# Kernel tuning notes

Measured on AMD Instinct MI355X. Metric: run time of the kernel, lower is better.

## Reference

```python
import jax, jax.numpy as jnp
import numpy as np

B, N, I, D, K = 64, 16, 2048, 32, 32  # batch, num_capsule, input_num_capsule, dim_capsule, input_dim_capsule
ROUTINGS = 3
EPS = 1e-07


def squash(s):
    # squared_norm includes per-element eps before the sum, matching torch code
    sq = jnp.sum(s * s + EPS, axis=-1, keepdims=True)
    return sq * s / ((1.0 + sq) * jnp.sqrt(sq))


def setup_inputs() -> dict:
    key = jax.random.key(0)
    kx, kw = jax.random.split(key)
    x = jax.random.normal(kx, (B, I, K), dtype=jnp.float32)
    # xavier_uniform over a [N, I, D, K] tensor: fan_in = D*K (last two dims treated as matrix by torch init? torch treats dim1.. as fan) -- use gain=1 uniform bound per torch's convention: fan_in = I*D*K/... Use simple xavier over (fan_in=K, fan_out=D) receptive field I*N.
    fan_in = I * K
    fan_out = I * D  # torch: fan_in = size(1)*receptive, here just use uniform bound from full-tensor xavier
    bound = float(np.sqrt(6.0 / (fan_in + fan_out)))
    W = jax.random.uniform(kw, (N, I, D, K), minval=-bound, maxval=bound, dtype=jnp.float32)
    return {"x": x, "W": W}


def reference(x, W):
    # u_hat[b,n,i,d] = sum_k W[n,i,d,k] * x[b,i,k]
    u_hat = jnp.einsum('nidk,bik->bnid', W, x)
    b = jnp.zeros((B, N, I), dtype=u_hat.dtype)
    v = None
    for r in range(ROUTINGS):
        c = jax.nn.softmax(b, axis=1)                 # softmax over num_capsule
        s = jnp.einsum('bni,bnid->bnd', c, u_hat)     # [B, N, D]
        v = squash(s)
        if r < ROUTINGS - 1:
            a = jnp.einsum('bnid,bnd->bni', u_hat, v)
            b = b + a
    return v  # [B, N, D]
```

## Files before the change

### kernel.cpp

```cpp
#include <hip/hip_runtime.h>
#include <stdint.h>

#define Bdim 64
#define Ndim 16
#define Idim 2048
#define Ddim 32
#define Kdim 32
#define EPSV 1e-7f

#define TILE_I   4
#define TILES_PB 16
#define NB_Y     (Idim / (TILE_I * TILES_PB))

typedef __attribute__((ext_vector_type(8))) short short8v;
typedef __attribute__((ext_vector_type(4))) float f32x4;

static __device__ __forceinline__ unsigned pk_rne(float a, float b) {
    unsigned ua = __float_as_uint(a);
    unsigned ub = __float_as_uint(b);
    ua = (ua + 0x7fffu + ((ua >> 16) & 1u)) >> 16;
    ub = (ub + 0x7fffu + ((ub >> 16) & 1u)) >> 16;
    return (ua & 0xffffu) | (ub << 16);
}
static __device__ __forceinline__ float bf2f(unsigned us) {
    return __uint_as_float(us << 16);
}

#define GLL16(g, s)                                                              \
    __builtin_amdgcn_global_load_lds(                                            \
        (const __attribute__((address_space(1))) void*)(uintptr_t)(const void*)(g), \
        (__attribute__((address_space(3))) void*)(uintptr_t)(void*)(s), 16, 0, 0)

__global__ __launch_bounds__(256) void convert_x(
    const float* __restrict__ x, unsigned short* __restrict__ x2)
{
    const int i  = blockIdx.x;
    const int b  = threadIdx.x >> 2;
    const int ko = threadIdx.x & 3;
    const float* src = x + ((size_t)b * Idim + i) * Kdim + (ko << 3);
    float4 a = ((const float4*)src)[0];
    float4 c = ((const float4*)src)[1];
    uint4 o;
    o.x = pk_rne(a.x, a.y); o.y = pk_rne(a.z, a.w);
    o.z = pk_rne(c.x, c.y); o.w = pk_rne(c.z, c.w);
    *(uint4*)(x2 + ((size_t)i * 64 + b) * 32 + (ko << 3)) = o;
}

__global__ __launch_bounds__(256) void pass1_dma(
    const float* __restrict__ W, const unsigned short* __restrict__ x2,
    unsigned short* __restrict__ uhat, float* __restrict__ s0)
{
    __shared__ float          ldsW[2][TILE_I * 1024];
    __shared__ unsigned short ldsX[2][TILE_I * 2048];

    const int n     = blockIdx.x;
    const int iblk0 = blockIdx.y * (TILE_I * TILES_PB);
    const int tid   = threadIdx.x;
    const int l     = tid & 63;
    const int bcol  = ((tid >> 6) << 4) + (l & 15);
    const int krow  = l >> 4;

    const float*          Wblk = W  + ((size_t)n * Idim + iblk0) * (Ddim * Kdim);
    const unsigned short* Xblk = x2 + (size_t)iblk0 * (64 * 32);

    f32x4 acc0 = {0.f, 0.f, 0.f, 0.f};
    f32x4 acc1 = {0.f, 0.f, 0.f, 0.f};
    const f32x4 zero = {0.f, 0.f, 0.f, 0.f};

    auto stage = [&](int t, int buf) {
        const float* Wt = Wblk + (size_t)t * (TILE_I * 1024);
        float* dw = &ldsW[buf][0];
        #pragma unroll
        for (int j = 0; j < 4; ++j) {
            const int c  = j * 256 + tid;
            const int lc = c & 63, h = (c >> 6) & 1, mt = (c >> 7) & 1, il = c >> 8;
            const float* src = Wt + il * 1024 + ((mt << 4) + (lc & 15)) * 32
                                  + ((lc >> 4) << 3) + (h << 2);
            GLL16(src, dw + (size_t)c * 4);
        }
        const unsigned short* Xt = Xblk + (size_t)t * (TILE_I * 2048);
        unsigned short* dx = &ldsX[buf][0];
        #pragma unroll
        for (int j = 0; j < 4; ++j) {
            const int c = j * 256 + tid;
            GLL16(Xt + (size_t)c * 8, dx + (size_t)c * 8);
        }
    };

    stage(0, 0);

    for (int t = 0; t < TILES_PB; ++t) {
        if (t + 1 < TILES_PB) stage(t + 1, (t + 1) & 1);
        if (t == 0 || t == TILES_PB - 1) {
            asm volatile("s_waitcnt vmcnt(8)" ::: "memory");
        } else {
            asm volatile("s_waitcnt vmcnt(16)" ::: "memory");
        }
        __builtin_amdgcn_s_barrier();
        __builtin_amdgcn_sched_barrier(0);

        const float*          lw = &ldsW[t & 1][0];
        const unsigned short* lx = &ldsX[t & 1][0];
        const int ibase = iblk0 + t * TILE_I;

        #pragma unroll
        for (int il = 0; il < TILE_I; ++il) {
            const int i = ibase + il;

            union { short8v v; unsigned u[4]; } bf, af0, af1;
            bf.v = *(const short8v*)(lx + il * 2048 + bcol * 32 + (krow << 3));

            const float4 w00 = *(const float4*)(lw + ((il * 256 + l)       << 2));
            const float4 w01 = *(const float4*)(lw + ((il * 256 + 64 + l)  << 2));
            const float4 w10 = *(const float4*)(lw + ((il * 256 + 128 + l) << 2));
            const float4 w11 = *(const float4*)(lw + ((il * 256 + 192 + l) << 2));
            af0.u[0] = pk_rne(w00.x, w00.y); af0.u[1] = pk_rne(w00.z, w00.w);
            af0.u[2] = pk_rne(w01.x, w01.y); af0.u[3] = pk_rne(w01.z, w01.w);
            af1.u[0] = pk_rne(w10.x, w10.y); af1.u[1] = pk_rne(w10.z, w10.w);
            af1.u[2] = pk_rne(w11.x, w11.y); af1.u[3] = pk_rne(w11.z, w11.w);

            f32x4 c0 = __builtin_amdgcn_mfma_f32_16x16x32_bf16(af0.v, bf.v, zero, 0, 0, 0);
            f32x4 c1 = __builtin_amdgcn_mfma_f32_16x16x32_bf16(af1.v, bf.v, zero, 0, 0, 0);

            const size_t ubase = (((size_t)i * Ndim + n) * 64 + bcol) * Ddim + (krow << 2);
            uint2 p0; p0.x = pk_rne(c0[0], c0[1]); p0.y = pk_rne(c0[2], c0[3]);
            *(uint2*)(uhat + ubase) = p0;
            uint2 p1; p1.x = pk_rne(c1[0], c1[1]); p1.y = pk_rne(c1[2], c1[3]);
            *(uint2*)(uhat + ubase + 16) = p1;

            acc0 += c0;
            acc1 += c1;
        }
        asm volatile("s_waitcnt lgkmcnt(0)" ::: "memory");
        __builtin_amdgcn_s_barrier();
        __builtin_amdgcn_sched_barrier(0);
    }

    float* sp = s0 + ((size_t)bcol * Ndim + n) * Ddim + (krow << 2);
    #pragma unroll
    for (int r = 0; r < 4; ++r) atomicAdd(sp + r, acc0[r]);
    #pragma unroll
    for (int r = 0; r < 4; ++r) atomicAdd(sp + 16 + r, acc1[r]);
}

__global__ __launch_bounds__(256) void pass1_simple(
    const float* __restrict__ W, const float* __restrict__ x,
    unsigned short* __restrict__ uhat, float* __restrict__ s0, int bbase, int Bc)
{
    const int IB = 16;
    const int n  = blockIdx.x;
    const int i0 = blockIdx.y * IB;
    const int w  = threadIdx.x >> 6;
    const int l  = threadIdx.x & 63;
    const int bcol  = (w << 4) + (l & 15);
    const int bglob = bbase + bcol;
    const int krow  = l >> 4;

    f32x4 acc0 = {0.f,0.f,0.f,0.f}, acc1 = {0.f,0.f,0.f,0.f};
    const f32x4 zero = {0.f,0.f,0.f,0.f};

    for (int ii = 0; ii < IB; ++ii) {
        const int i = i0 + ii;
        const float* xp = x + ((size_t)bglob * Idim + i) * Kdim + (krow << 3);
        float4 xa = ((const float4*)xp)[0];
        float4 xb = ((const float4*)xp)[1];
        union { short8v v; unsigned u[4]; } bf, af0, af1;
        bf.u[0]=pk_rne(xa.x,xa.y); bf.u[1]=pk_rne(xa.z,xa.w);
        bf.u[2]=pk_rne(xb.x,xb.y); bf.u[3]=pk_rne(xb.z,xb.w);

        const float* wbase = W + ((size_t)n * Idim + i) * Ddim * Kdim + (krow << 3);
        const float* wp0 = wbase + (size_t)(l & 15) * Kdim;
        float4 wa = ((const float4*)wp0)[0];
        float4 wb = ((const float4*)wp0)[1];
        af0.u[0]=pk_rne(wa.x,wa.y); af0.u[1]=pk_rne(wa.z,wa.w);
        af0.u[2]=pk_rne(wb.x,wb.y); af0.u[3]=pk_rne(wb.z,wb.w);
        const float* wp1 = wp0 + 16 * Kdim;
        float4 wc = ((const float4*)wp1)[0];
        float4 wd = ((const float4*)wp1)[1];
        af1.u[0]=pk_rne(wc.x,wc.y); af1.u[1]=pk_rne(wc.z,wc.w);
        af1.u[2]=pk_rne(wd.x,wd.y); af1.u[3]=pk_rne(wd.z,wd.w);

        f32x4 c0 = __builtin_amdgcn_mfma_f32_16x16x32_bf16(af0.v, bf.v, zero, 0,0,0);
        f32x4 c1 = __builtin_amdgcn_mfma_f32_16x16x32_bf16(af1.v, bf.v, zero, 0,0,0);

        const size_t ubase = (((size_t)i * Ndim + n) * Bc + bcol) * Ddim + (krow << 2);
        uint2 p0; p0.x=pk_rne(c0[0],c0[1]); p0.y=pk_rne(c0[2],c0[3]);
        *(uint2*)(uhat + ubase) = p0;
        uint2 p1; p1.x=pk_rne(c1[0],c1[1]); p1.y=pk_rne(c1[2],c1[3]);
        *(uint2*)(uhat + ubase + 16) = p1;
        acc0 += c0; acc1 += c1;
    }
    float* sp = s0 + ((size_t)bglob * Ndim + n) * Ddim + (krow << 2);
    #pragma unroll
    for (int r = 0; r < 4; ++r) atomicAdd(sp + r, acc0[r]);
    #pragma unroll
    for (int r = 0; r < 4; ++r) atomicAdd(sp + 16 + r, acc1[r]);
}

template<int FIRST>
__global__ __launch_bounds__(256) void route_kernel(
    const unsigned short* __restrict__ uhat, const float* __restrict__ vin,
    float* __restrict__ bbuf, float* __restrict__ sout, int bbase, int Bc)
{
    const int bc = blockIdx.x;
    const int it = blockIdx.y;
    const int w = threadIdx.x >> 6;
    const int l = threadIdx.x & 63;
    const int g = l >> 2, q = l & 3;
    const int bglob = bbase + bc;

    const float* vp = vin + ((size_t)bglob * Ndim + g) * Ddim + (q << 3);
    float vreg[8];
    *(float4*)&vreg[0] = ((const float4*)vp)[0];
    *(float4*)&vreg[4] = ((const float4*)vp)[1];

    float sacc[8];
    #pragma unroll
    for (int j = 0; j < 8; ++j) sacc[j] = 0.f;

    for (int base = 0; base < 128; base += 16) {
        const int i0v = (it << 7) + base + w;

        uint4 ur[4];
        float bl[4];
        #pragma unroll
        for (int j = 0; j < 4; ++j) {
            const int i = i0v + 4 * j;
            ur[j] = *(const uint4*)(uhat + (((size_t)i * Ndim + g) * Bc + bc) * Ddim + (q << 3));
            if (!FIRST) bl[j] = bbuf[((size_t)bc * Idim + i) * Ndim + g];
        }

        #pragma unroll
        for (int j = 0; j < 4; ++j) {
            const int i = i0v + 4 * j;
            float u[8];
            u[0] = bf2f(ur[j].x & 0xffffu); u[1] = bf2f(ur[j].x >> 16);
            u[2] = bf2f(ur[j].y & 0xffffu); u[3] = bf2f(ur[j].y >> 16);
            u[4] = bf2f(ur[j].z & 0xffffu); u[5] = bf2f(ur[j].z >> 16);
            u[6] = bf2f(ur[j].w & 0xffffu); u[7] = bf2f(ur[j].w >> 16);

            float p = 0.f;
            #pragma unroll
            for (int k = 0; k < 8; ++k) p = fmaf(u[k], vreg[k], p);
            p += __shfl_xor(p, 1);
            p += __shfl_xor(p, 2);

            float logit = p;
            if (FIRST) {
                if (q == 0) bbuf[((size_t)bc * Idim + i) * Ndim + g] = p;
            } else {
                logit += bl[j];
            }
            float m = logit;
            m = fmaxf(m, __shfl_xor(m, 4));
            m = fmaxf(m, __shfl_xor(m, 8));
            m = fmaxf(m, __shfl_xor(m, 16));
            m = fmaxf(m, __shfl_xor(m, 32));
            float e = __expf(logit - m);
            float z = e;
            z += __shfl_xor(z, 4);
            z += __shfl_xor(z, 8);
            z += __shfl_xor(z, 16);
            z += __shfl_xor(z, 32);
            float c = e / z;

            #pragma unroll
            for (int k = 0; k < 8; ++k) sacc[k] = fmaf(c, u[k], sacc[k]);
        }
    }

    __shared__ float sl[4][512];
    #pragma unroll
    for (int j = 0; j < 8; ++j) sl[w][(l << 3) + j] = sacc[j];
    __syncthreads();
    for (int e2 = threadIdx.x; e2 < 512; e2 += 256) {
        float vsum = sl[0][e2] + sl[1][e2] + sl[2][e2] + sl[3][e2];
        atomicAdd(sout + (size_t)bglob * (Ndim * Ddim) + e2, vsum);
    }
}

__global__ __launch_bounds__(256) void squash_kernel(
    const float* __restrict__ s, float* __restrict__ vout, float scale, int bbase)
{
    const int tid = blockIdx.x * 256 + threadIdx.x;
    const int row = tid >> 5;
    const int d   = tid & 31;
    const size_t off = ((size_t)bbase * Ndim + row) * Ddim + d;
    float sv = s[off] * scale;
    float t = fmaf(sv, sv, EPSV);
    t += __shfl_xor(t, 1);
    t += __shfl_xor(t, 2);
    t += __shfl_xor(t, 4);
    t += __shfl_xor(t, 8);
    t += __shfl_xor(t, 16);
    float vv = sv * t / ((1.f + t) * sqrtf(t));
    vout[off] = vv;
}

extern "C" void kernel_launch(void* const* d_in, const int* in_sizes, int n_in,
                              void* d_out, int out_size, void* d_ws, size_t ws_size,
                              hipStream_t stream)
{
    (void)in_sizes; (void)n_in; (void)out_size;
    const float* x = (const float*)d_in[0];
    const float* W = (const float*)d_in[1];
    float* out = (float*)d_out;

    const size_t snd = (size_t)Bdim * Ndim * Ddim;
    const size_t fixed = 5 * snd * sizeof(float);

    int Bc = 64;
    while (Bc > 16) {
        size_t need = (size_t)Bc * Idim * Ndim * Ddim * 2 + (size_t)Bc * Idim * Ndim * 4 + fixed;
        if (need <= ws_size) break;
        Bc >>= 1;
    }

    char* p = (char*)d_ws;
    unsigned short* uhat = (unsigned short*)p; p += (size_t)Bc * Idim * Ndim * Ddim * 2;
    float* bbuf = (float*)p;                   p += (size_t)Bc * Idim * Ndim * 4;
    float* sbuf = (float*)p;
    float* s0 = sbuf;
    float* s1 = sbuf + snd;
    float* s2 = sbuf + 2 * snd;
    float* v0 = sbuf + 3 * snd;
    float* v1 = sbuf + 4 * snd;

    for (int bbase = 0; bbase < Bdim; bbase += Bc) {
        (void)hipMemsetAsync(sbuf, 0, 3 * snd * sizeof(float), stream);

        if (Bc == 64) {
            unsigned short* x2 = (unsigned short*)bbuf;
            convert_x<<<dim3(Idim), 256, 0, stream>>>(x, x2);
            pass1_dma<<<dim3(Ndim, NB_Y), 256, 0, stream>>>(W, x2, uhat, s0);
        } else {
            pass1_simple<<<dim3(Ndim, Idim / 16), dim3(64 * (Bc / 16)), 0, stream>>>(
                W, x, uhat, s0, bbase, Bc);
        }
        squash_kernel<<<dim3(Bc * 2), 256, 0, stream>>>(s0, v0, 1.f / 16.f, bbase);

        route_kernel<1><<<dim3(Bc, Idim / 128), 256, 0, stream>>>(uhat, v0, bbuf, s1, bbase, Bc);
        squash_kernel<<<dim3(Bc * 2), 256, 0, stream>>>(s1, v1, 1.f, bbase);

        route_kernel<0><<<dim3(Bc, Idim / 128), 256, 0, stream>>>(uhat, v1, bbuf, s2, bbase, Bc);
        squash_kernel<<<dim3(Bc * 2), 256, 0, stream>>>(s2, out, 1.f, bbase);
    }
}
```

Measured before the change: 175.6 us.

## Deepen pass1 DMA pipeline to four buffers and restructure routing thread mapping

The pass1 kernel now uses smaller i-tiles (2 instead of 4) with a four-deep LDS ring and three tiles of prefetch, adjusting the vmcnt waits to match. The aim is to hide more global-load latency per block. The routing kernel is remapped so each lane owns a whole capsule (all 32 d values) for one i. This removes the intra-quad dot-product shuffles and the max-reduction, drops the softmax max subtraction and swaps the division for a reciprocal. The trade-offs are higher register pressure (64+ floats per lane), wider per-lane loads and possible overflow in exp without max subtraction.

```diff
diff --git a/kernel.cpp b/kernel.cpp
--- a/kernel.cpp
+++ b/kernel.cpp
@@ -8,9 +8,10 @@
 #define Kdim 32
 #define EPSV 1e-7f
 
-#define TILE_I   4
-#define TILES_PB 16
+#define TILE_I   2
+#define TILES_PB 32
 #define NB_Y     (Idim / (TILE_I * TILES_PB))
+#define NBUF     4
 
 typedef __attribute__((ext_vector_type(8))) short short8v;
 typedef __attribute__((ext_vector_type(4))) float f32x4;
@@ -24,6 +25,12 @@
 }
 static __device__ __forceinline__ float bf2f(unsigned us) {
     return __uint_as_float(us << 16);
+}
+static __device__ __forceinline__ void unpack8(uint4 r, float* u) {
+    u[0] = bf2f(r.x & 0xffffu); u[1] = bf2f(r.x >> 16);
+    u[2] = bf2f(r.y & 0xffffu); u[3] = bf2f(r.y >> 16);
+    u[4] = bf2f(r.z & 0xffffu); u[5] = bf2f(r.z >> 16);
+    u[6] = bf2f(r.w & 0xffffu); u[7] = bf2f(r.w >> 16);
 }
 
 #define GLL16(g, s)                                                              \
@@ -50,8 +57,8 @@
     const float* __restrict__ W, const unsigned short* __restrict__ x2,
     unsigned short* __restrict__ uhat, float* __restrict__ s0)
 {
-    __shared__ float          ldsW[2][TILE_I * 1024];
-    __shared__ unsigned short ldsX[2][TILE_I * 2048];
+    __shared__ float          ldsW[NBUF][TILE_I * 1024];
+    __shared__ unsigned short ldsX[NBUF][TILE_I * 2048];
 
     const int n     = blockIdx.x;
     const int iblk0 = blockIdx.y * (TILE_I * TILES_PB);
@@ -67,11 +74,12 @@
     f32x4 acc1 = {0.f, 0.f, 0.f, 0.f};
     const f32x4 zero = {0.f, 0.f, 0.f, 0.f};
 
-    auto stage = [&](int t, int buf) {
+    auto stage = [&](int t) {
+        const int buf = t & (NBUF - 1);
         const float* Wt = Wblk + (size_t)t * (TILE_I * 1024);
         float* dw = &ldsW[buf][0];
         #pragma unroll
-        for (int j = 0; j < 4; ++j) {
+        for (int j = 0; j < 2; ++j) {
             const int c  = j * 256 + tid;
             const int lc = c & 63, h = (c >> 6) & 1, mt = (c >> 7) & 1, il = c >> 8;
             const float* src = Wt + il * 1024 + ((mt << 4) + (lc & 15)) * 32
@@ -81,26 +89,30 @@
         const unsigned short* Xt = Xblk + (size_t)t * (TILE_I * 2048);
         unsigned short* dx = &ldsX[buf][0];
         #pragma unroll
-        for (int j = 0; j < 4; ++j) {
+        for (int j = 0; j < 2; ++j) {
             const int c = j * 256 + tid;
             GLL16(Xt + (size_t)c * 8, dx + (size_t)c * 8);
         }
     };
 
-    stage(0, 0);
+    stage(0); stage(1); stage(2);
 
     for (int t = 0; t < TILES_PB; ++t) {
-        if (t + 1 < TILES_PB) stage(t + 1, (t + 1) & 1);
+        if (t + 3 < TILES_PB) stage(t + 3);
         if (t == 0 || t == TILES_PB - 1) {
-            asm volatile("s_waitcnt vmcnt(8)" ::: "memory");
+            asm volatile("s_waitcnt vmcnt(12)" ::: "memory");
+        } else if (t == 1 || t == TILES_PB - 2) {
+            asm volatile("s_waitcnt vmcnt(16)" ::: "memory");
+        } else if (t == 2 || t == TILES_PB - 3) {
+            asm volatile("s_waitcnt vmcnt(20)" ::: "memory");
         } else {
-            asm volatile("s_waitcnt vmcnt(16)" ::: "memory");
+            asm volatile("s_waitcnt vmcnt(24)" ::: "memory");
         }
         __builtin_amdgcn_s_barrier();
         __builtin_amdgcn_sched_barrier(0);
 
-        const float*          lw = &ldsW[t & 1][0];
-        const unsigned short* lx = &ldsX[t & 1][0];
+        const float*          lw = &ldsW[t & (NBUF - 1)][0];
+        const unsigned short* lx = &ldsX[t & (NBUF - 1)][0];
         const int ibase = iblk0 + t * TILE_I;
 
         #pragma unroll
@@ -204,78 +216,78 @@
 {
     const int bc = blockIdx.x;
     const int it = blockIdx.y;
-    const int w = threadIdx.x >> 6;
-    const int l = threadIdx.x & 63;
-    const int g = l >> 2, q = l & 3;
+    const int w  = threadIdx.x >> 6;
+    const int l  = threadIdx.x & 63;
+    const int g    = l & 15;
+    const int iloc = l >> 4;
     const int bglob = bbase + bc;
 
-    const float* vp = vin + ((size_t)bglob * Ndim + g) * Ddim + (q << 3);
-    float vreg[8];
-    *(float4*)&vreg[0] = ((const float4*)vp)[0];
-    *(float4*)&vreg[4] = ((const float4*)vp)[1];
-
-    float sacc[8];
-    #pragma unroll
-    for (int j = 0; j < 8; ++j) sacc[j] = 0.f;
-
-    for (int base = 0; base < 128; base += 16) {
-        const int i0v = (it << 7) + base + w;
-
-        uint4 ur[4];
-        float bl[4];
-        #pragma unroll
-        for (int j = 0; j < 4; ++j) {
-            const int i = i0v + 4 * j;
-            ur[j] = *(const uint4*)(uhat + (((size_t)i * Ndim + g) * Bc + bc) * Ddim + (q << 3));
-            if (!FIRST) bl[j] = bbuf[((size_t)bc * Idim + i) * Ndim + g];
-        }
-
-        #pragma unroll
-        for (int j = 0; j < 4; ++j) {
-            const int i = i0v + 4 * j;
-            float u[8];
-            u[0] = bf2f(ur[j].x & 0xffffu); u[1] = bf2f(ur[j].x >> 16);
-            u[2] = bf2f(ur[j].y & 0xffffu); u[3] = bf2f(ur[j].y >> 16);
-            u[4] = bf2f(ur[j].z & 0xffffu); u[5] = bf2f(ur[j].z >> 16);
-            u[6] = bf2f(ur[j].w & 0xffffu); u[7] = bf2f(ur[j].w >> 16);
-
-            float p = 0.f;
-            #pragma unroll
-            for (int k = 0; k < 8; ++k) p = fmaf(u[k], vreg[k], p);
-            p += __shfl_xor(p, 1);
-            p += __shfl_xor(p, 2);
-
-            float logit = p;
-            if (FIRST) {
-                if (q == 0) bbuf[((size_t)bc * Idim + i) * Ndim + g] = p;
-            } else {
-                logit += bl[j];
-            }
-            float m = logit;
-            m = fmaxf(m, __shfl_xor(m, 4));
-            m = fmaxf(m, __shfl_xor(m, 8));
-            m = fmaxf(m, __shfl_xor(m, 16));
-            m = fmaxf(m, __shfl_xor(m, 32));
-            float e = __expf(logit - m);
-            float z = e;
-            z += __shfl_xor(z, 4);
-            z += __shfl_xor(z, 8);
-            z += __shfl_xor(z, 16);
-            z += __shfl_xor(z, 32);
-            float c = e / z;
-
-            #pragma unroll
-            for (int k = 0; k < 8; ++k) sacc[k] = fmaf(c, u[k], sacc[k]);
-        }
+    float v[32];
+    {
+        const float* vp = vin + ((size_t)bglob * Ndim + g) * Ddim;
+        #pragma unroll
+        for (int r = 0; r < 8; ++r) *(float4*)&v[r * 4] = ((const float4*)vp)[r];
+    }
+
+    float sacc[32];
+    #pragma unroll
+    for (int d = 0; d < 32; ++d) sacc[d] = 0.f;
+
+    const int ibase0 = (it << 7) + (w << 5);
+    for (int j = 0; j < 8; ++j) {
+        const int i = ibase0 + (j << 2) + iloc;
+        const unsigned short* up = uhat + (((size_t)i * Ndim + g) * Bc + bc) * Ddim;
+        const uint4 r0 = ((const uint4*)up)[0];
+        const uint4 r1 = ((const uint4*)up)[1];
+        const uint4 r2 = ((const uint4*)up)[2];
+        const uint4 r3 = ((const uint4*)up)[3];
+        float u[32];
+        unpack8(r0, u + 0); unpack8(r1, u + 8); unpack8(r2, u + 16); unpack8(r3, u + 24);
+
+        float a0 = 0.f, a1 = 0.f, a2 = 0.f, a3 = 0.f;
+        #pragma unroll
+        for (int d = 0; d < 32; d += 4) {
+            a0 = fmaf(u[d + 0], v[d + 0], a0);
+            a1 = fmaf(u[d + 1], v[d + 1], a1);
+            a2 = fmaf(u[d + 2], v[d + 2], a2);
+            a3 = fmaf(u[d + 3], v[d + 3], a3);
+        }
+        const float a = (a0 + a1) + (a2 + a3);
+
+        const size_t boff = (((size_t)bc * Idim + ibase0 + (j << 2)) << 4) + l;
+        float logit = a;
+        if (FIRST) {
+            bbuf[boff] = a;
+        } else {
+            logit += bbuf[boff];
+        }
+        float e = __expf(logit);
+        float z = e;
+        z += __shfl_xor(z, 1);
+        z += __shfl_xor(z, 2);
+        z += __shfl_xor(z, 4);
+        z += __shfl_xor(z, 8);
+        const float c = e * __builtin_amdgcn_rcpf(z);
+
+        #pragma unroll
+        for (int d = 0; d < 32; ++d) sacc[d] = fmaf(c, u[d], sacc[d]);
+    }
+
+    #pragma unroll
+    for (int d = 0; d < 32; ++d) {
+        sacc[d] += __shfl_xor(sacc[d], 16);
+        sacc[d] += __shfl_xor(sacc[d], 32);
     }
 
     __shared__ float sl[4][512];
-    #pragma unroll
-    for (int j = 0; j < 8; ++j) sl[w][(l << 3) + j] = sacc[j];
+    if (iloc == 0) {
+        #pragma unroll
+        for (int d = 0; d < 32; ++d) sl[w][(g << 5) + d] = sacc[d];
+    }
     __syncthreads();
     for (int e2 = threadIdx.x; e2 < 512; e2 += 256) {
-        float vsum = sl[0][e2] + sl[1][e2] + sl[2][e2] + sl[3][e2];
-        atomicAdd(sout + (size_t)bglob * (Ndim * Ddim) + e2, vsum);
+        float vs = sl[0][e2] + sl[1][e2] + sl[2][e2] + sl[3][e2];
+        atomicAdd(sout + (size_t)bglob * (Ndim * Ddim) + e2, vs);
     }
 }
 
```

New measurement: 200.3 us. 1.14x slower.
